# Kernel optimization log

Hardware: AMD Instinct MI355X
Metric: run time of the kernel (lower is better)

The kernel has to match this reference:

```python
import jax, jax.numpy as jnp
import numpy as np

EPS = 1e-5
NUM_HEADS = 8

def _conv(x, w, stride=1, pad='VALID'):
    if isinstance(pad, int):
        pad = [(pad, pad), (pad, pad)]
    return jax.lax.conv_general_dilated(x, w, (stride, stride), pad,
                                        dimension_numbers=('NCHW', 'OIHW', 'NCHW'))

def _bn_relu(x, g, b):
    # eval-mode BatchNorm2d with running_mean=0, running_var=1 (fresh-module stats)
    scale = g / np.sqrt(1.0 + EPS)
    return jax.nn.relu(x * scale[None, :, None, None] + b[None, :, None, None])

def _patch_embed(x, w1, w23, bn, proj_w, proj_b):
    # stem: 7x7 s1 -> BN+ReLU -> 3x3 -> BN+ReLU -> 3x3 -> BN+ReLU (Dropout2d is identity in eval)
    x = _bn_relu(_conv(x, w1, 1, 3), bn[0, 0], bn[0, 1])
    x = _bn_relu(_conv(x, w23[0], 1, 1), bn[1, 0], bn[1, 1])
    x = _bn_relu(_conv(x, w23[1], 1, 1), bn[2, 0], bn[2, 1])
    # proj: 8x8 conv stride 8 -> (B,192,28,28)
    return _conv(x, proj_w, 8, 'VALID') + proj_b[None, :, None, None]

def _mha(qx, kx, vx, qkv_w, qkv_b, o_w, o_b):
    B, C, H, W = qx.shape
    hd = C // NUM_HEADS
    def proj(x, w, b):
        y = jnp.einsum('oc,bchw->bohw', w, x) + b[None, :, None, None]
        return y.reshape(B, NUM_HEADS, hd, H, W)
    q = proj(qx, qkv_w[0], qkv_b[0])
    k = proj(kx, qkv_w[1], qkv_b[1])
    v = proj(vx, qkv_w[2], qkv_b[2])
    # faithful to torch.matmul on 5D (B,heads,head_dim,H,W): contraction over W, softmax over k's H axis
    logits = jnp.einsum('bndhw,bndgw->bndhg', q, k) / jnp.sqrt(jnp.float32(W))
    attn = jax.nn.softmax(logits, axis=-1)
    out = jnp.einsum('bndhg,bndgw->bndhw', attn, v).reshape(B, C, H, W)
    return jnp.einsum('oc,bchw->bohw', o_w, out) + o_b[None, :, None, None]

def reference(face, body,
              f_w1, f_w23, f_bn, f_proj_w, f_proj_b,
              b_w1, b_w23, b_bn, b_proj_w, b_proj_b,
              a1_qkv_w, a1_qkv_b, a1_o_w, a1_o_b,
              a2_qkv_w, a2_qkv_b, a2_o_w, a2_o_b,
              cov_w, cov_bn_g, cov_bn_b):
    f = _patch_embed(face, f_w1, f_w23, f_bn, f_proj_w, f_proj_b)   # (B,192,28,28)
    b = _patch_embed(body, b_w1, b_w23, b_bn, b_proj_w, b_proj_b)   # (B,192,28,28)
    f_out = _mha(f, b, b, a1_qkv_w, a1_qkv_b, a1_o_w, a1_o_b)
    b_out = _mha(b, f, f, a2_qkv_w, a2_qkv_b, a2_o_w, a2_o_b)
    cat = jnp.concatenate([f_out, b_out], axis=1)                    # (B,384,28,28)
    y = jnp.einsum('oc,bchw->bohw', cov_w, cat)                      # 1x1 conv, no bias
    return _bn_relu(y, cov_bn_g, cov_bn_b)                           # (B,192,28,28)

def setup_inputs() -> dict:
    key = jax.random.key(0)
    ks = iter(jax.random.split(key, 40))
    s = 0.05
    r = lambda shape: jax.random.normal(next(ks), shape, jnp.float32)
    d = {}
    d['face'] = r((16, 3, 224, 224))
    d['body'] = r((16, 3, 224, 224))
    for p in ('f', 'b'):
        d[p + '_w1'] = r((64, 3, 7, 7)) * s
        d[p + '_w23'] = r((2, 64, 64, 3, 3)) * s
        d[p + '_bn'] = jnp.stack([1.0 + 0.1 * r((3, 64)), 0.1 * r((3, 64))], axis=1)  # (3,2,64)
        d[p + '_proj_w'] = r((192, 64, 8, 8)) * s
        d[p + '_proj_b'] = r((192,)) * s
    for a in ('a1', 'a2'):
        d[a + '_qkv_w'] = r((3, 192, 192)) * s
        d[a + '_qkv_b'] = r((3, 192)) * s
        d[a + '_o_w'] = r((192, 192)) * s
        d[a + '_o_b'] = r((192,)) * s
    d['cov_w'] = r((192, 384)) * s
    d['cov_bn_g'] = 1.0 + 0.1 * r((192,))
    d['cov_bn_b'] = 0.1 * r((192,))
    return d
```

## Files before the change

### kernel.cpp

```cpp
#include <hip/hip_runtime.h>
#include <hip/hip_bf16.h>
#include <math.h>

#define BATCH 16
#define H1 224
#define C1 64
#define HP 28
#define P2 784
#define C2 192
#define NQ ((size_t)BATCH*C2*P2)
#define CHW ((size_t)C1*H1*H1)
#define W3SZ 23040
#define WPSZ 786432

typedef __attribute__((ext_vector_type(8))) short short8;
typedef __attribute__((ext_vector_type(4))) short s16x4;
typedef __attribute__((ext_vector_type(4))) float f32x4;

__device__ __forceinline__ ushort f2bf(float v) {
  __hip_bfloat16 h = __float2bfloat16(v);
  return *(ushort*)&h;
}

__global__ __launch_bounds__(256) void wprep3(
    const float* __restrict__ fw, const float* __restrict__ bw,
    ushort* __restrict__ dst)
{
  int e = blockIdx.x * 256 + threadIdx.x;
  if (e >= 184320) return;
  int i = e % 40;
  int r = e / 40;
  int t = r % 9; r /= 9;
  int o = r % 64; r /= 64;
  int c = r % 2; r /= 2;
  int l = r % 2; int s = r / 2;
  float v = 0.f;
  if (i < 32) {
    const float* wsrc = s ? bw : fw;
    v = wsrc[l * 36864 + o * 576 + (c * 32 + i) * 9 + t];
  }
  dst[e] = f2bf(v);
}

__global__ __launch_bounds__(256) void cast_bf16(
    const float* __restrict__ src, ushort* __restrict__ dst, int n)
{
  int i = blockIdx.x * 256 + threadIdx.x;
  if (i < n) dst[i] = f2bf(src[i]);
}

__global__ __launch_bounds__(256) void conv7_mfma(
    const float* __restrict__ x, const float* __restrict__ w,
    const float* __restrict__ bn, ushort* __restrict__ out)
{
  __shared__ ushort in_lds[22 * 160];
  __shared__ ushort w_lds[64 * 232];
  int tid = threadIdx.x;
  int wv = tid >> 6, lane = tid & 63;
  int l15 = lane & 15, q = lane >> 4;
  int x0 = blockIdx.x * 32, y0 = blockIdx.y * 16;
  int b = blockIdx.z;

  for (int k = tid; k < 3520; k += 256) {
    int i = k & 3;
    int t = k >> 2;
    int col = t % 40, row = t / 40;
    int gy = y0 - 3 + row, gx = x0 - 3 + col;
    float v = 0.0f;
    if (i < 3 && col < 38 && gy >= 0 && gy < H1 && gx >= 0 && gx < H1)
      v = x[((size_t)(b * 3 + i) * H1 + gy) * H1 + gx];
    in_lds[row * 160 + col * 4 + i] = f2bf(v);
  }
  for (int k = tid; k < 14336; k += 256) {
    int och = k / 224;
    int rem = k - och * 224;
    int dy = rem >> 5, kk = rem & 31;
    int dx = kk >> 2, i = kk & 3;
    float v = 0.0f;
    if (i < 3 && dx < 7) v = w[och * 147 + i * 49 + dy * 7 + dx];
    w_lds[och * 232 + dy * 32 + kk] = f2bf(v);
  }
  __syncthreads();

  f32x4 acc[4][8];
  #pragma unroll
  for (int m = 0; m < 4; m++)
    #pragma unroll
    for (int n = 0; n < 8; n++) acc[m][n] = (f32x4){0.f, 0.f, 0.f, 0.f};

  #pragma unroll
  for (int dy = 0; dy < 7; dy++) {
    short8 afr[4];
    #pragma unroll
    for (int m = 0; m < 4; m++)
      afr[m] = *(const short8*)&w_lds[(m * 16 + l15) * 232 + dy * 32 + q * 8];
    #pragma unroll
    for (int n = 0; n < 8; n++) {
      int r = 4 * wv + (n >> 1) + dy;
      int c = (n & 1) * 16 + l15;
      int e = r * 160 + c * 4 + q * 8;
      s16x4 lo = *(const s16x4*)&in_lds[e];
      s16x4 hi = *(const s16x4*)&in_lds[e + 4];
      short8 bfr = __builtin_shufflevector(lo, hi, 0, 1, 2, 3, 4, 5, 6, 7);
      #pragma unroll
      for (int m = 0; m < 4; m++)
        acc[m][n] = __builtin_amdgcn_mfma_f32_16x16x32_bf16(
            afr[m], bfr, acc[m][n], 0, 0, 0);
    }
  }

  const float inv = 1.0f / sqrtf(1.0f + 1e-5f);
  #pragma unroll
  for (int m = 0; m < 4; m++) {
    #pragma unroll
    for (int n = 0; n < 8; n++) {
      int py = y0 + 4 * wv + (n >> 1);
      int px = x0 + (n & 1) * 16 + l15;
      #pragma unroll
      for (int j = 0; j < 4; j++) {
        int och = m * 16 + q * 4 + j;
        float sc = bn[och] * inv, be = bn[64 + och];
        float v = fmaxf(acc[m][n][j] * sc + be, 0.0f);
        out[((size_t)(b * C1 + och) * H1 + py) * H1 + px] = f2bf(v);
      }
    }
  }
}

__global__ __launch_bounds__(256) void conv3_mfma(
    const ushort* __restrict__ x, const ushort* __restrict__ wp,
    const float* __restrict__ bn, ushort* __restrict__ out)
{
  __shared__ ushort in_lds[10][34][40];
  __shared__ ushort w_lds[W3SZ];
  int tid = threadIdx.x;
  int wv = tid >> 6, lane = tid & 63;
  int l15 = lane & 15, q = lane >> 4;
  int x0 = blockIdx.x * 32, y0 = blockIdx.y * 8;
  int b = blockIdx.z;

  f32x4 acc[4][4];
  #pragma unroll
  for (int m = 0; m < 4; m++)
    #pragma unroll
    for (int n = 0; n < 4; n++) acc[m][n] = (f32x4){0.f, 0.f, 0.f, 0.f};

  for (int ic = 0; ic < 2; ic++) {
    int ich0 = ic * 32;
    __syncthreads();
    for (int oct = tid; oct < 1360; oct += 256) {
      int o8 = oct / 340;
      int t = oct - o8 * 340;
      int c = t % 34, r = t / 34;
      int gy = y0 - 1 + r, gx = x0 - 1 + c;
      short8 v = (short8){0, 0, 0, 0, 0, 0, 0, 0};
      if (gy >= 0 && gy < H1 && gx >= 0 && gx < H1) {
        const ushort* sp = x + ((size_t)(b * C1 + ich0 + o8 * 8) * H1 + gy) * H1 + gx;
        #pragma unroll
        for (int j = 0; j < 8; j++) v[j] = (short)sp[(size_t)j * H1 * H1];
      }
      *(short8*)&in_lds[r][c][o8 * 8] = v;
    }
    {
      const ushort* wsrc = wp + ic * W3SZ;
      for (int f = tid; f < 2880; f += 256)
        *(short8*)&w_lds[f * 8] = *(const short8*)&wsrc[f * 8];
    }
    __syncthreads();
    #pragma unroll
    for (int dy = 0; dy < 3; dy++) {
      #pragma unroll
      for (int dx = 0; dx < 3; dx++) {
        int tap = dy * 3 + dx;
        short8 afr[4];
        #pragma unroll
        for (int m = 0; m < 4; m++)
          afr[m] = *(const short8*)&w_lds[(m * 16 + l15) * 360 + tap * 40 + q * 8];
        short8 bfr[4];
        #pragma unroll
        for (int n = 0; n < 4; n++) {
          int r = 2 * wv + (n >> 1) + dy;
          int c = (n & 1) * 16 + l15 + dx;
          bfr[n] = *(const short8*)&in_lds[r][c][q * 8];
        }
        #pragma unroll
        for (int m = 0; m < 4; m++)
          #pragma unroll
          for (int n = 0; n < 4; n++)
            acc[m][n] = __builtin_amdgcn_mfma_f32_16x16x32_bf16(
                afr[m], bfr[n], acc[m][n], 0, 0, 0);
      }
    }
  }
  const float inv = 1.0f / sqrtf(1.0f + 1e-5f);
  #pragma unroll
  for (int m = 0; m < 4; m++) {
    #pragma unroll
    for (int n = 0; n < 4; n++) {
      int py = y0 + 2 * wv + (n >> 1);
      int px = x0 + (n & 1) * 16 + l15;
      #pragma unroll
      for (int j = 0; j < 4; j++) {
        int och = m * 16 + q * 4 + j;
        float sc = bn[och] * inv, be = bn[64 + och];
        float v = fmaxf(acc[m][n][j] * sc + be, 0.0f);
        out[((size_t)(b * C1 + och) * H1 + py) * H1 + px] = f2bf(v);
      }
    }
  }
}

__global__ __launch_bounds__(256) void proj8_mfma(
    const ushort* __restrict__ x, const ushort* __restrict__ wp,
    const float* __restrict__ bias, float* __restrict__ out)
{
  __shared__ ushort a_lds[64 * 136];
  __shared__ ushort b_lds[64 * 136];
  int tid = threadIdx.x;
  int wv = tid >> 6, lane = tid & 63;
  int l15 = lane & 15, q = lane >> 4;
  int wm = wv >> 1, wn = wv & 1;
  int p0 = blockIdx.x * 64, o0 = blockIdx.y * 64;
  int b = blockIdx.z;

  f32x4 acc[2][2];
  #pragma unroll
  for (int m = 0; m < 2; m++)
    #pragma unroll
    for (int n = 0; n < 2; n++) acc[m][n] = (f32x4){0.f, 0.f, 0.f, 0.f};

  for (int ic0 = 0; ic0 < 64; ic0 += 2) {
    __syncthreads();
    for (int f = tid; f < 1024; f += 256) {
      int oo = f >> 4, r8 = f & 15;
      *(short8*)&a_lds[oo * 136 + r8 * 8] =
          *(const short8*)&wp[(size_t)(o0 + oo) * 4096 + ic0 * 64 + r8 * 8];
    }
    for (int f = tid; f < 1024; f += 256) {
      int pp = f & 63, rr = f >> 6;
      int ic = rr >> 3, dy = rr & 7;
      int p = p0 + pp;
      short8 v = (short8){0, 0, 0, 0, 0, 0, 0, 0};
      if (p < P2) {
        int py = p / 28, px = p - 28 * py;
        v = *(const short8*)&x[((size_t)(b * C1 + ic0 + ic) * H1 + 8 * py + dy) * H1 + 8 * px];
      }
      *(short8*)&b_lds[pp * 136 + ic * 64 + dy * 8] = v;
    }
    __syncthreads();
    #pragma unroll
    for (int ks = 0; ks < 4; ks++) {
      short8 afr[2], bfr[2];
      #pragma unroll
      for (int m = 0; m < 2; m++)
        afr[m] = *(const short8*)&a_lds[(wm * 32 + m * 16 + l15) * 136 + ks * 32 + q * 8];
      #pragma unroll
      for (int n = 0; n < 2; n++)
        bfr[n] = *(const short8*)&b_lds[(wn * 32 + n * 16 + l15) * 136 + ks * 32 + q * 8];
      #pragma unroll
      for (int m = 0; m < 2; m++)
        #pragma unroll
        for (int n = 0; n < 2; n++)
          acc[m][n] = __builtin_amdgcn_mfma_f32_16x16x32_bf16(
              afr[m], bfr[n], acc[m][n], 0, 0, 0);
    }
  }
  #pragma unroll
  for (int m = 0; m < 2; m++) {
    #pragma unroll
    for (int n = 0; n < 2; n++) {
      int p = p0 + wn * 32 + n * 16 + l15;
      if (p >= P2) continue;
      #pragma unroll
      for (int j = 0; j < 4; j++) {
        int o = o0 + wm * 32 + m * 16 + q * 4 + j;
        out[((size_t)(b * C2 + o)) * P2 + p] = acc[m][n][j] + bias[o];
      }
    }
  }
}

__global__ __launch_bounds__(256) void qkv192(
    const float* __restrict__ xq, const float* __restrict__ xkv,
    const float* __restrict__ w, const float* __restrict__ bias,
    float* __restrict__ out)
{
  int p = blockIdx.x * 256 + threadIdx.x;
  if (p >= P2) return;
  int by = blockIdx.y;
  int which = by / 48, o0 = (by % 48) * 4;
  int b = blockIdx.z;
  const float* xp = (which == 0 ? xq : xkv) + (size_t)b * C2 * P2 + p;
  const float* wp = w + (size_t)which * C2 * C2 + (size_t)o0 * C2;
  float a0 = bias[which * C2 + o0 + 0];
  float a1 = bias[which * C2 + o0 + 1];
  float a2 = bias[which * C2 + o0 + 2];
  float a3 = bias[which * C2 + o0 + 3];
  #pragma unroll 8
  for (int c = 0; c < C2; c++) {
    float xv = xp[(size_t)c * P2];
    a0 = fmaf(wp[c], xv, a0);
    a1 = fmaf(wp[C2 + c], xv, a1);
    a2 = fmaf(wp[2 * C2 + c], xv, a2);
    a3 = fmaf(wp[3 * C2 + c], xv, a3);
  }
  float* op = out + (size_t)which * NQ + ((size_t)b * C2 + o0) * P2 + p;
  op[0] = a0; op[P2] = a1; op[2 * P2] = a2; op[3 * P2] = a3;
}

__global__ __launch_bounds__(256) void attn_core(
    const float* __restrict__ qkv, float* __restrict__ out)
{
  __shared__ __align__(16) float qs[P2], ks[P2], vs[P2];
  __shared__ __align__(16) float As[28][29];
  int c = blockIdx.x, b = blockIdx.y;
  int tid = threadIdx.x;
  size_t base = ((size_t)b * C2 + c) * P2;
  const float* Q = qkv + base;
  const float* K = qkv + NQ + base;
  const float* V = qkv + 2 * NQ + base;
  for (int idx = tid; idx < P2; idx += 256) {
    qs[idx] = Q[idx]; ks[idx] = K[idx]; vs[idx] = V[idx];
  }
  __syncthreads();
  const float scl = 1.0f / sqrtf(28.0f);
  for (int idx = tid; idx < P2; idx += 256) {
    int h = idx / 28, g = idx - 28 * h;
    float s = 0.f;
    #pragma unroll
    for (int ww = 0; ww < 28; ww++) s = fmaf(qs[h * 28 + ww], ks[g * 28 + ww], s);
    As[h][g] = s * scl;
  }
  __syncthreads();
  if (tid < 28) {
    float m = -1e30f;
    #pragma unroll
    for (int g = 0; g < 28; g++) m = fmaxf(m, As[tid][g]);
    float sum = 0.f;
    #pragma unroll
    for (int g = 0; g < 28; g++) {
      float e = expf(As[tid][g] - m);
      As[tid][g] = e;
      sum += e;
    }
    float r = 1.0f / sum;
    #pragma unroll
    for (int g = 0; g < 28; g++) As[tid][g] *= r;
  }
  __syncthreads();
  for (int idx = tid; idx < P2; idx += 256) {
    int h = idx / 28, ww = idx - 28 * h;
    float s = 0.f;
    #pragma unroll
    for (int g = 0; g < 28; g++) s = fmaf(As[h][g], vs[g * 28 + ww], s);
    out[base + idx] = s;
  }
}

__global__ __launch_bounds__(256) void pw192(
    const float* __restrict__ x, const float* __restrict__ w,
    const float* __restrict__ bias, float* __restrict__ out)
{
  int p = blockIdx.x * 256 + threadIdx.x;
  if (p >= P2) return;
  int o0 = blockIdx.y * 4;
  int b = blockIdx.z;
  const float* xp = x + (size_t)b * C2 * P2 + p;
  const float* wp = w + (size_t)o0 * C2;
  float a0 = bias[o0 + 0], a1 = bias[o0 + 1], a2 = bias[o0 + 2], a3 = bias[o0 + 3];
  #pragma unroll 8
  for (int c = 0; c < C2; c++) {
    float xv = xp[(size_t)c * P2];
    a0 = fmaf(wp[c], xv, a0);
    a1 = fmaf(wp[C2 + c], xv, a1);
    a2 = fmaf(wp[2 * C2 + c], xv, a2);
    a3 = fmaf(wp[3 * C2 + c], xv, a3);
  }
  float* op = out + ((size_t)b * C2 + o0) * P2 + p;
  op[0] = a0; op[P2] = a1; op[2 * P2] = a2; op[3 * P2] = a3;
}

__global__ __launch_bounds__(256) void cov_bnrelu(
    const float* __restrict__ fo, const float* __restrict__ bo,
    const float* __restrict__ w, const float* __restrict__ g,
    const float* __restrict__ be, float* __restrict__ out)
{
  int p = blockIdx.x * 256 + threadIdx.x;
  if (p >= P2) return;
  int o0 = blockIdx.y * 4;
  int b = blockIdx.z;
  float a[4] = {0.f, 0.f, 0.f, 0.f};
  const float* wp = w + (size_t)o0 * 384;
  const float* xp = fo + (size_t)b * C2 * P2 + p;
  #pragma unroll 8
  for (int c = 0; c < C2; c++) {
    float xv = xp[(size_t)c * P2];
    #pragma unroll
    for (int oo = 0; oo < 4; oo++) a[oo] = fmaf(wp[oo * 384 + c], xv, a[oo]);
  }
  xp = bo + (size_t)b * C2 * P2 + p;
  #pragma unroll 8
  for (int c = 0; c < C2; c++) {
    float xv = xp[(size_t)c * P2];
    #pragma unroll
    for (int oo = 0; oo < 4; oo++) a[oo] = fmaf(wp[oo * 384 + 192 + c], xv, a[oo]);
  }
  const float inv = 1.0f / sqrtf(1.0f + 1e-5f);
  #pragma unroll
  for (int oo = 0; oo < 4; oo++) {
    int o = o0 + oo;
    out[((size_t)b * C2 + o) * P2 + p] = fmaxf(a[oo] * (g[o] * inv) + be[o], 0.0f);
  }
}

extern "C" void kernel_launch(void* const* d_in, const int* in_sizes, int n_in,
                              void* d_out, int out_size, void* d_ws, size_t ws_size,
                              hipStream_t stream) {
  (void)in_sizes; (void)n_in; (void)out_size;
  const float* face = (const float*)d_in[0];
  const float* body = (const float*)d_in[1];
  const float* f_w1 = (const float*)d_in[2];
  const float* f_w23 = (const float*)d_in[3];
  const float* f_bn = (const float*)d_in[4];
  const float* f_pw = (const float*)d_in[5];
  const float* f_pb = (const float*)d_in[6];
  const float* b_w1 = (const float*)d_in[7];
  const float* b_w23 = (const float*)d_in[8];
  const float* b_bn = (const float*)d_in[9];
  const float* b_pw = (const float*)d_in[10];
  const float* b_pb = (const float*)d_in[11];
  const float* a1_qkv_w = (const float*)d_in[12];
  const float* a1_qkv_b = (const float*)d_in[13];
  const float* a1_o_w = (const float*)d_in[14];
  const float* a1_o_b = (const float*)d_in[15];
  const float* a2_qkv_w = (const float*)d_in[16];
  const float* a2_qkv_b = (const float*)d_in[17];
  const float* a2_o_w = (const float*)d_in[18];
  const float* a2_o_b = (const float*)d_in[19];
  const float* cov_w = (const float*)d_in[20];
  const float* cov_g = (const float*)d_in[21];
  const float* cov_b = (const float*)d_in[22];
  float* out = (float*)d_out;

  size_t availF = ws_size / sizeof(float);
  const size_t preF = 92160 + 786432;
  int ck = 2;
  for (int cand = 16; cand >= 4; cand >>= 1) {
    size_t bigF = (size_t)cand * CHW;
    if (bigF < 6 * NQ) bigF = 6 * NQ;
    if (2 * NQ + preF + bigF <= availF) { ck = cand; break; }
  }

  float* ws = (float*)d_ws;
  float* embf = ws;
  float* embb = ws + NQ;
  ushort* wpre3 = (ushort*)(ws + 2 * NQ);
  ushort* wpreP = (ushort*)(ws + 2 * NQ + 92160);
  float* big = ws + 2 * NQ + preF;
  ushort* sb0 = (ushort*)big;
  ushort* sb1 = (ushort*)big + (size_t)ck * CHW;
  float* qkv = big;
  float* att = big + 3 * NQ;
  float* fo  = big + 4 * NQ;
  float* bo  = big + 5 * NQ;

  wprep3<<<720, 256, 0, stream>>>(f_w23, b_w23, wpre3);
  cast_bf16<<<(WPSZ + 255) / 256, 256, 0, stream>>>(f_pw, wpreP, WPSZ);
  cast_bf16<<<(WPSZ + 255) / 256, 256, 0, stream>>>(b_pw, wpreP + WPSZ, WPSZ);

  for (int c0 = 0; c0 < BATCH; c0 += ck) {
    const float* xin = face + (size_t)c0 * 3 * H1 * H1;
    conv7_mfma<<<dim3(7, 14, ck), 256, 0, stream>>>(xin, f_w1, f_bn, sb0);
    conv3_mfma<<<dim3(7, 28, ck), 256, 0, stream>>>(sb0, wpre3, f_bn + 128, sb1);
    conv3_mfma<<<dim3(7, 28, ck), 256, 0, stream>>>(sb1, wpre3 + 2 * W3SZ, f_bn + 256, sb0);
    proj8_mfma<<<dim3(13, 3, ck), 256, 0, stream>>>(sb0, wpreP, f_pb, embf + (size_t)c0 * C2 * P2);
  }

  for (int c0 = 0; c0 < BATCH; c0 += ck) {
    const float* xin = body + (size_t)c0 * 3 * H1 * H1;
    conv7_mfma<<<dim3(7, 14, ck), 256, 0, stream>>>(xin, b_w1, b_bn, sb0);
    conv3_mfma<<<dim3(7, 28, ck), 256, 0, stream>>>(sb0, wpre3 + 4 * W3SZ, b_bn + 128, sb1);
    conv3_mfma<<<dim3(7, 28, ck), 256, 0, stream>>>(sb1, wpre3 + 6 * W3SZ, b_bn + 256, sb0);
    proj8_mfma<<<dim3(13, 3, ck), 256, 0, stream>>>(sb0, wpreP + WPSZ, b_pb, embb + (size_t)c0 * C2 * P2);
  }

  qkv192<<<dim3(4, 144, BATCH), 256, 0, stream>>>(embf, embb, a1_qkv_w, a1_qkv_b, qkv);
  attn_core<<<dim3(C2, BATCH), 256, 0, stream>>>(qkv, att);
  pw192<<<dim3(4, 48, BATCH), 256, 0, stream>>>(att, a1_o_w, a1_o_b, fo);

  qkv192<<<dim3(4, 144, BATCH), 256, 0, stream>>>(embb, embf, a2_qkv_w, a2_qkv_b, qkv);
  attn_core<<<dim3(C2, BATCH), 256, 0, stream>>>(qkv, att);
  pw192<<<dim3(4, 48, BATCH), 256, 0, stream>>>(att, a2_o_w, a2_o_b, bo);

  cov_bnrelu<<<dim3(4, 48, BATCH), 256, 0, stream>>>(fo, bo, cov_w, cov_g, cov_b, out);
}
```

Before: 1.465 ms.

## Replace scalar pointwise GEMMs with bf16 MFMA kernels and swizzle conv3 blocks

Replaces the scalar FP32 QKV, output-projection and final 1x1-conv kernels with LDS-tiled bf16 MFMA GEMM kernels using 64x64 output tiles. The final one fuses BN+ReLU. This is meant to cut ALU and redundant global loads in the attention tail. It also remaps conv3 workgroup indices with a stride-8 swizzle, likely to spread neighbouring tiles across XCDs/caches. It adds bf16 rounding of activations and weights, and the swizzle assumes the block count divides evenly by 8.

```diff
diff --git a/kernel.cpp b/kernel.cpp
--- a/kernel.cpp
+++ b/kernel.cpp
@@ -136,8 +136,14 @@
   int tid = threadIdx.x;
   int wv = tid >> 6, lane = tid & 63;
   int l15 = lane & 15, q = lane >> 4;
-  int x0 = blockIdx.x * 32, y0 = blockIdx.y * 8;
-  int b = blockIdx.z;
+
+  int flat = blockIdx.x + 7 * (blockIdx.y + 28 * blockIdx.z);
+  int nwg = 196 * gridDim.z;
+  int swz = (flat & 7) * (nwg >> 3) + (flat >> 3);
+  int x0 = (swz % 7) * 32;
+  int t0 = swz / 7;
+  int y0 = (t0 % 28) * 8;
+  int b = t0 / 28;
 
   f32x4 acc[4][4];
   #pragma unroll
@@ -280,32 +286,157 @@
   }
 }
 
-__global__ __launch_bounds__(256) void qkv192(
-    const float* __restrict__ xq, const float* __restrict__ xkv,
+__global__ __launch_bounds__(256) void pw_mfma(
+    const float* __restrict__ Xq, const float* __restrict__ Xkv,
     const float* __restrict__ w, const float* __restrict__ bias,
     float* __restrict__ out)
 {
-  int p = blockIdx.x * 256 + threadIdx.x;
-  if (p >= P2) return;
-  int by = blockIdx.y;
-  int which = by / 48, o0 = (by % 48) * 4;
+  __shared__ ushort a_lds[64 * 200];
+  __shared__ ushort b_lds[64 * 200];
+  int tid = threadIdx.x;
+  int wv = tid >> 6, lane = tid & 63;
+  int l15 = lane & 15, q = lane >> 4;
+  int wm = wv >> 1, wn = wv & 1;
+  int p0 = blockIdx.x * 64;
+  int which = blockIdx.y / 3, o0 = (blockIdx.y % 3) * 64;
   int b = blockIdx.z;
-  const float* xp = (which == 0 ? xq : xkv) + (size_t)b * C2 * P2 + p;
-  const float* wp = w + (size_t)which * C2 * C2 + (size_t)o0 * C2;
-  float a0 = bias[which * C2 + o0 + 0];
-  float a1 = bias[which * C2 + o0 + 1];
-  float a2 = bias[which * C2 + o0 + 2];
-  float a3 = bias[which * C2 + o0 + 3];
-  #pragma unroll 8
-  for (int c = 0; c < C2; c++) {
-    float xv = xp[(size_t)c * P2];
-    a0 = fmaf(wp[c], xv, a0);
-    a1 = fmaf(wp[C2 + c], xv, a1);
-    a2 = fmaf(wp[2 * C2 + c], xv, a2);
-    a3 = fmaf(wp[3 * C2 + c], xv, a3);
-  }
-  float* op = out + (size_t)which * NQ + ((size_t)b * C2 + o0) * P2 + p;
-  op[0] = a0; op[P2] = a1; op[2 * P2] = a2; op[3 * P2] = a3;
+  const float* X = (which == 0 ? Xq : Xkv) + (size_t)b * C2 * P2;
+  const float* wp = w + (size_t)which * C2 * C2;
+
+  for (int f = tid; f < 1536; f += 256) {
+    int oo = f / 24, k8 = f % 24;
+    const float* src = wp + (size_t)(o0 + oo) * C2 + k8 * 8;
+    ushort* dst = &a_lds[oo * 200 + k8 * 8];
+    #pragma unroll
+    for (int j = 0; j < 8; j++) dst[j] = f2bf(src[j]);
+  }
+  for (int f = tid; f < 1536; f += 256) {
+    int pp = f & 63, c8 = f >> 6;
+    int p = p0 + pp;
+    short8 v = (short8){0, 0, 0, 0, 0, 0, 0, 0};
+    if (p < P2) {
+      #pragma unroll
+      for (int j = 0; j < 8; j++)
+        v[j] = (short)f2bf(X[(size_t)(c8 * 8 + j) * P2 + p]);
+    }
+    *(short8*)&b_lds[pp * 200 + c8 * 8] = v;
+  }
+  __syncthreads();
+
+  f32x4 acc[2][2];
+  #pragma unroll
+  for (int m = 0; m < 2; m++)
+    #pragma unroll
+    for (int n = 0; n < 2; n++) acc[m][n] = (f32x4){0.f, 0.f, 0.f, 0.f};
+
+  #pragma unroll
+  for (int ks = 0; ks < 6; ks++) {
+    short8 afr[2], bfr[2];
+    #pragma unroll
+    for (int m = 0; m < 2; m++)
+      afr[m] = *(const short8*)&a_lds[(wm * 32 + m * 16 + l15) * 200 + ks * 32 + q * 8];
+    #pragma unroll
+    for (int n = 0; n < 2; n++)
+      bfr[n] = *(const short8*)&b_lds[(wn * 32 + n * 16 + l15) * 200 + ks * 32 + q * 8];
+    #pragma unroll
+    for (int m = 0; m < 2; m++)
+      #pragma unroll
+      for (int n = 0; n < 2; n++)
+        acc[m][n] = __builtin_amdgcn_mfma_f32_16x16x32_bf16(
+            afr[m], bfr[n], acc[m][n], 0, 0, 0);
+  }
+
+  float* op = out + (size_t)which * NQ + (size_t)b * C2 * P2;
+  #pragma unroll
+  for (int m = 0; m < 2; m++) {
+    #pragma unroll
+    for (int n = 0; n < 2; n++) {
+      int p = p0 + wn * 32 + n * 16 + l15;
+      if (p >= P2) continue;
+      #pragma unroll
+      for (int j = 0; j < 4; j++) {
+        int o = o0 + wm * 32 + m * 16 + q * 4 + j;
+        op[(size_t)o * P2 + p] = acc[m][n][j] + bias[which * C2 + o];
+      }
+    }
+  }
+}
+
+__global__ __launch_bounds__(256) void cov_mfma(
+    const float* __restrict__ fo, const float* __restrict__ bo,
+    const float* __restrict__ w, const float* __restrict__ g,
+    const float* __restrict__ be, float* __restrict__ out)
+{
+  __shared__ ushort a_lds[64 * 200];
+  __shared__ ushort b_lds[64 * 200];
+  int tid = threadIdx.x;
+  int wv = tid >> 6, lane = tid & 63;
+  int l15 = lane & 15, q = lane >> 4;
+  int wm = wv >> 1, wn = wv & 1;
+  int p0 = blockIdx.x * 64, o0 = blockIdx.y * 64;
+  int b = blockIdx.z;
+
+  f32x4 acc[2][2];
+  #pragma unroll
+  for (int m = 0; m < 2; m++)
+    #pragma unroll
+    for (int n = 0; n < 2; n++) acc[m][n] = (f32x4){0.f, 0.f, 0.f, 0.f};
+
+  for (int cc = 0; cc < 2; cc++) {
+    const float* X = (cc ? bo : fo) + (size_t)b * C2 * P2;
+    __syncthreads();
+    for (int f = tid; f < 1536; f += 256) {
+      int oo = f / 24, k8 = f % 24;
+      const float* src = w + (size_t)(o0 + oo) * 384 + cc * C2 + k8 * 8;
+      ushort* dst = &a_lds[oo * 200 + k8 * 8];
+      #pragma unroll
+      for (int j = 0; j < 8; j++) dst[j] = f2bf(src[j]);
+    }
+    for (int f = tid; f < 1536; f += 256) {
+      int pp = f & 63, c8 = f >> 6;
+      int p = p0 + pp;
+      short8 v = (short8){0, 0, 0, 0, 0, 0, 0, 0};
+      if (p < P2) {
+        #pragma unroll
+        for (int j = 0; j < 8; j++)
+          v[j] = (short)f2bf(X[(size_t)(c8 * 8 + j) * P2 + p]);
+      }
+      *(short8*)&b_lds[pp * 200 + c8 * 8] = v;
+    }
+    __syncthreads();
+    #pragma unroll
+    for (int ks = 0; ks < 6; ks++) {
+      short8 afr[2], bfr[2];
+      #pragma unroll
+      for (int m = 0; m < 2; m++)
+        afr[m] = *(const short8*)&a_lds[(wm * 32 + m * 16 + l15) * 200 + ks * 32 + q * 8];
+      #pragma unroll
+      for (int n = 0; n < 2; n++)
+        bfr[n] = *(const short8*)&b_lds[(wn * 32 + n * 16 + l15) * 200 + ks * 32 + q * 8];
+      #pragma unroll
+      for (int m = 0; m < 2; m++)
+        #pragma unroll
+        for (int n = 0; n < 2; n++)
+          acc[m][n] = __builtin_amdgcn_mfma_f32_16x16x32_bf16(
+              afr[m], bfr[n], acc[m][n], 0, 0, 0);
+    }
+  }
+
+  const float inv = 1.0f / sqrtf(1.0f + 1e-5f);
+  #pragma unroll
+  for (int m = 0; m < 2; m++) {
+    #pragma unroll
+    for (int n = 0; n < 2; n++) {
+      int p = p0 + wn * 32 + n * 16 + l15;
+      if (p >= P2) continue;
+      #pragma unroll
+      for (int j = 0; j < 4; j++) {
+        int o = o0 + wm * 32 + m * 16 + q * 4 + j;
+        float v = fmaxf(acc[m][n][j] * (g[o] * inv) + be[o], 0.0f);
+        out[((size_t)b * C2 + o) * P2 + p] = v;
+      }
+    }
+  }
 }
 
 __global__ __launch_bounds__(256) void attn_core(
@@ -354,62 +485,6 @@
     #pragma unroll
     for (int g = 0; g < 28; g++) s = fmaf(As[h][g], vs[g * 28 + ww], s);
     out[base + idx] = s;
-  }
-}
-
-__global__ __launch_bounds__(256) void pw192(
-    const float* __restrict__ x, const float* __restrict__ w,
-    const float* __restrict__ bias, float* __restrict__ out)
-{
-  int p = blockIdx.x * 256 + threadIdx.x;
-  if (p >= P2) return;
-  int o0 = blockIdx.y * 4;
-  int b = blockIdx.z;
-  const float* xp = x + (size_t)b * C2 * P2 + p;
-  const float* wp = w + (size_t)o0 * C2;
-  float a0 = bias[o0 + 0], a1 = bias[o0 + 1], a2 = bias[o0 + 2], a3 = bias[o0 + 3];
-  #pragma unroll 8
-  for (int c = 0; c < C2; c++) {
-    float xv = xp[(size_t)c * P2];
-    a0 = fmaf(wp[c], xv, a0);
-    a1 = fmaf(wp[C2 + c], xv, a1);
-    a2 = fmaf(wp[2 * C2 + c], xv, a2);
-    a3 = fmaf(wp[3 * C2 + c], xv, a3);
-  }
-  float* op = out + ((size_t)b * C2 + o0) * P2 + p;
-  op[0] = a0; op[P2] = a1; op[2 * P2] = a2; op[3 * P2] = a3;
-}
-
-__global__ __launch_bounds__(256) void cov_bnrelu(
-    const float* __restrict__ fo, const float* __restrict__ bo,
-    const float* __restrict__ w, const float* __restrict__ g,
-    const float* __restrict__ be, float* __restrict__ out)
-{
-  int p = blockIdx.x * 256 + threadIdx.x;
-  if (p >= P2) return;
-  int o0 = blockIdx.y * 4;
-  int b = blockIdx.z;
-  float a[4] = {0.f, 0.f, 0.f, 0.f};
-  const float* wp = w + (size_t)o0 * 384;
-  const float* xp = fo + (size_t)b * C2 * P2 + p;
-  #pragma unroll 8
-  for (int c = 0; c < C2; c++) {
-    float xv = xp[(size_t)c * P2];
-    #pragma unroll
-    for (int oo = 0; oo < 4; oo++) a[oo] = fmaf(wp[oo * 384 + c], xv, a[oo]);
-  }
-  xp = bo + (size_t)b * C2 * P2 + p;
-  #pragma unroll 8
-  for (int c = 0; c < C2; c++) {
-    float xv = xp[(size_t)c * P2];
-    #pragma unroll
-    for (int oo = 0; oo < 4; oo++) a[oo] = fmaf(wp[oo * 384 + 192 + c], xv, a[oo]);
-  }
-  const float inv = 1.0f / sqrtf(1.0f + 1e-5f);
-  #pragma unroll
-  for (int oo = 0; oo < 4; oo++) {
-    int o = o0 + oo;
-    out[((size_t)b * C2 + o) * P2 + p] = fmaxf(a[oo] * (g[o] * inv) + be[o], 0.0f);
   }
 }
 
@@ -484,13 +559,13 @@
     proj8_mfma<<<dim3(13, 3, ck), 256, 0, stream>>>(sb0, wpreP + WPSZ, b_pb, embb + (size_t)c0 * C2 * P2);
   }
 
-  qkv192<<<dim3(4, 144, BATCH), 256, 0, stream>>>(embf, embb, a1_qkv_w, a1_qkv_b, qkv);
+  pw_mfma<<<dim3(13, 9, BATCH), 256, 0, stream>>>(embf, embb, a1_qkv_w, a1_qkv_b, qkv);
   attn_core<<<dim3(C2, BATCH), 256, 0, stream>>>(qkv, att);
-  pw192<<<dim3(4, 48, BATCH), 256, 0, stream>>>(att, a1_o_w, a1_o_b, fo);
-
-  qkv192<<<dim3(4, 144, BATCH), 256, 0, stream>>>(embb, embf, a2_qkv_w, a2_qkv_b, qkv);
+  pw_mfma<<<dim3(13, 3, BATCH), 256, 0, stream>>>(att, att, a1_o_w, a1_o_b, fo);
+
+  pw_mfma<<<dim3(13, 9, BATCH), 256, 0, stream>>>(embb, embf, a2_qkv_w, a2_qkv_b, qkv);
   attn_core<<<dim3(C2, BATCH), 256, 0, stream>>>(qkv, att);
-  pw192<<<dim3(4, 48, BATCH), 256, 0, stream>>>(att, a2_o_w, a2_o_b, bo);
-
-  cov_bnrelu<<<dim3(4, 48, BATCH), 256, 0, stream>>>(fo, bo, cov_w, cov_g, cov_b, out);
-}
+  pw_mfma<<<dim3(13, 3, BATCH), 256, 0, stream>>>(att, att, a2_o_w, a2_o_b, bo);
+
+  cov_mfma<<<dim3(13, 3, BATCH), 256, 0, stream>>>(fo, bo, cov_w, cov_g, cov_b, out);
+}
```

Result: faster. 1.220 ms (-16.7%).
